# Kernel tuning notes

Measured on AMD Instinct MI355X. Metric: run time of the kernel, lower is better.

Reference implementation:

```python
import jax, jax.numpy as jnp
import numpy as np

N, C, H, W = 4, 128, 64, 64
HEADS, KS, RED = 4, 7, 18
D = C // HEADS


def _layernorm(x, w, b, eps=1e-5):
    mu = x.mean(axis=-1, keepdims=True)
    var = ((x - mu) ** 2).mean(axis=-1, keepdims=True)
    return (x - mu) * jax.lax.rsqrt(var + eps) * w + b


def _gelu(x):
    return jax.nn.gelu(x, approximate=False)


def setup_inputs() -> dict:
    key = jax.random.key(0)
    ks = jax.random.split(key, 16)
    s = 0.02
    inp = {
        'x': jax.random.normal(ks[0], (N, C, H, W), jnp.float32),
        'ln1_w': jnp.ones((C,), jnp.float32), 'ln1_b': jnp.zeros((C,), jnp.float32),
        'ln2_w': jnp.ones((C,), jnp.float32), 'ln2_b': jnp.zeros((C,), jnp.float32),
        'qkv_w': jax.random.normal(ks[1], (C, 3 * C), jnp.float32) * s,
        'qkv_b': jnp.zeros((3 * C,), jnp.float32),
        'proj_w': jax.random.normal(ks[2], (C, C), jnp.float32) * s,
        'proj_b': jnp.zeros((C,), jnp.float32),
        'rpb': jax.random.normal(ks[3], (HEADS, 2 * KS - 1, 2 * KS - 1), jnp.float32) * s,
        'conv1_w': jax.random.normal(ks[4], (C, C // 4), jnp.float32) * s,
        'conv1_b': jnp.zeros((C // 4,), jnp.float32),
        'conv2_w': jax.random.normal(ks[5], (C // 4, C), jnp.float32) * s,
        'conv2_b': jnp.zeros((C,), jnp.float32),
        'ca1_w': jax.random.normal(ks[6], (C, C // RED), jnp.float32) * s,
        'ca1_b': jnp.zeros((C // RED,), jnp.float32),
        'ca2_w': jax.random.normal(ks[7], (C // RED, C), jnp.float32) * s,
        'ca2_b': jnp.zeros((C,), jnp.float32),
        'fc1_w': jax.random.normal(ks[8], (C, 4 * C), jnp.float32) * s,
        'fc1_b': jnp.zeros((4 * C,), jnp.float32),
        'fc2_w': jax.random.normal(ks[9], (4 * C, C), jnp.float32) * s,
        'fc2_b': jnp.zeros((C,), jnp.float32),
    }
    return inp


def _na2d(xc, qkv_w, qkv_b, rpb, proj_w, proj_b):
    # xc: [N, H, W, C] -> neighborhood attention with clamped k x k windows (NATTEN semantics)
    n, h, w, c = xc.shape
    qkv = (xc @ qkv_w + qkv_b).reshape(n, h, w, 3, HEADS, D)
    q, k, v = qkv[..., 0, :, :], qkv[..., 1, :, :], qkv[..., 2, :, :]
    q = q * (D ** -0.5)
    half = KS // 2
    ni = jnp.clip(jnp.arange(h) - half, 0, h - KS)          # window start per query row
    nj = jnp.clip(jnp.arange(w) - half, 0, w - KS)
    idx_i = ni[:, None] + jnp.arange(KS)                     # [H, KS]
    idx_j = nj[:, None] + jnp.arange(KS)                     # [W, KS]
    # gather key/value windows: [N, H, KS, W, KS, heads, D]
    kw = k[:, idx_i][:, :, :, idx_j]
    vw = v[:, idx_i][:, :, :, idx_j]
    attn = jnp.einsum('nijhd,niajbhd->nijhab', q, kw)        # [N,H,W,heads,KS,KS]
    bi = idx_i - jnp.arange(h)[:, None] + (KS - 1)           # rel-pos bias row index [H,KS]
    bj = idx_j - jnp.arange(w)[:, None] + (KS - 1)           # [W,KS]
    bias = rpb[:, bi][:, :, :, bj]                           # [heads,H,KS,W,KS]
    attn = attn + bias.transpose(1, 3, 0, 2, 4)[None]        # -> [1,H,W,heads,KS,KS]
    attn = jax.nn.softmax(attn.reshape(n, h, w, HEADS, KS * KS), axis=-1)
    attn = attn.reshape(n, h, w, HEADS, KS, KS)
    out = jnp.einsum('nijhab,niajbhd->nijhd', attn, vw).reshape(n, h, w, c)
    return out @ proj_w + proj_b


def reference(x, ln1_w, ln1_b, ln2_w, ln2_b, qkv_w, qkv_b, proj_w, proj_b, rpb,
              conv1_w, conv1_b, conv2_w, conv2_b, ca1_w, ca1_b, ca2_w, ca2_b,
              fc1_w, fc1_b, fc2_w, fc2_b):
    n, c, h, w = x.shape
    xs = x.transpose(0, 2, 3, 1).reshape(n, h * w, c)        # n (h w) c
    shortcut = xs
    xn = _layernorm(xs, ln1_w, ln1_b)
    xc = xn.reshape(n, h, w, c)
    # conv branch: 1x1 -> GELU -> 1x1 -> channel attention
    t = _gelu(xc @ conv1_w + conv1_b) @ conv2_w + conv2_b
    g = t.mean(axis=(1, 2))                                  # global avg pool [N,C]
    g = jax.nn.sigmoid(jax.nn.relu(g @ ca1_w + ca1_b) @ ca2_w + ca2_b)
    ca_x = (t * g[:, None, None, :]).reshape(n, h * w, c)
    # neighborhood attention branch
    na_x = _na2d(xc, qkv_w, qkv_b, rpb, proj_w, proj_b).reshape(n, h * w, c)
    x2 = shortcut + na_x + ca_x * 0.02
    m = _gelu(_layernorm(x2, ln2_w, ln2_b) @ fc1_w + fc1_b) @ fc2_w + fc2_b
    x3 = x2 + m
    return x3.reshape(n, h, w, c).transpose(0, 3, 1, 2)
```

## Files before the change

### kernel.cpp

```cpp
#include <hip/hip_runtime.h>
#include <hip/hip_bf16.h>
#include <math.h>

#define NB 4
#define CC 128
#define HH 64
#define WW 64
#define HEADS 4
#define KS 7
#define DD 32
#define HW 4096
#define MTOT 16384

typedef unsigned short BF;
typedef short short8 __attribute__((ext_vector_type(8)));
typedef float floatx4 __attribute__((ext_vector_type(4)));

__device__ __forceinline__ float gelu_f(float x) {
    return 0.5f * x * (1.0f + erff(x * 0.70710678118654752440f));
}

__device__ __forceinline__ BF f2bf(float f) {
    union { float f; unsigned u; } a; a.f = f;
    unsigned u = a.u;
    unsigned r = u + 0x7FFFu + ((u >> 16) & 1u);
    return (BF)(r >> 16);
}

__device__ __forceinline__ float bf2f(BF v) {
    return __uint_as_float(((unsigned)v) << 16);
}

#define LDK 40
#define LDK128 136

__global__ __launch_bounds__(256) void ln1t_kernel(
    const float* __restrict__ x, const float* __restrict__ w,
    const float* __restrict__ b, BF* __restrict__ out,
    float* __restrict__ part,
    const float* __restrict__ qkv_w, const float* __restrict__ conv1_w,
    const float* __restrict__ conv2_w, const float* __restrict__ proj_w,
    const float* __restrict__ fc1_w, const float* __restrict__ fc2_w,
    BF* __restrict__ qkvT, BF* __restrict__ c1T, BF* __restrict__ c2T,
    BF* __restrict__ projT2, BF* __restrict__ fc1T2, BF* __restrict__ fc2T2)
{
    const int blk = blockIdx.x;
    const int t  = threadIdx.x;

    if (blk >= 512) {
        for (int idx = (blk - 512) * 256 + t; idx < 204800; idx += 32768) {
            if (idx < 49152) {
                int l = idx, n = l >> 7, k = l & 127;
                qkvT[l] = f2bf(qkv_w[k * 384 + n]);
            } else if (idx < 53248) {
                int l = idx - 49152, n = l >> 7, k = l & 127;
                c1T[l] = f2bf(conv1_w[k * 32 + n]);
            } else if (idx < 57344) {
                int l = idx - 53248, n = l >> 5, k = l & 31;
                c2T[l] = f2bf(conv2_w[k * 128 + n]);
            } else if (idx < 73728) {
                int l = idx - 57344, kk = l & 31, n = (l >> 5) & 127, ks = l >> 12;
                projT2[l] = f2bf(proj_w[(ks * 32 + kk) * 128 + n]);
            } else if (idx < 139264) {
                int l = idx - 73728, kk = l & 31, n = (l >> 5) & 511, ks = l >> 14;
                fc1T2[l] = f2bf(fc1_w[(ks * 32 + kk) * 512 + n]);
            } else {
                int l = idx - 139264, kk = l & 31, n = (l >> 5) & 127, ks = l >> 12;
                fc2T2[l] = f2bf(fc2_w[(ks * 32 + kk) * 128 + n]);
            }
        }
        return;
    }

    __shared__ float xt[128][33];
    __shared__ float mus[32], rss[32];
    const int n  = blk >> 7;
    const int p0 = (blk & 127) * 32;
    if (blk < 4 && t < 128) part[blk * CC + t] = 0.f;

    {
        int pp = t & 31, c8 = t >> 5;
        #pragma unroll 4
        for (int it = 0; it < 16; it++) {
            int c = it * 8 + c8;
            xt[c][pp] = x[(size_t)(n * CC + c) * HW + p0 + pp];
        }
    }
    __syncthreads();
    {
        int pp2 = t >> 3, cb = t & 7;
        float s = 0.f;
        #pragma unroll
        for (int u = 0; u < 16; u++) s += xt[cb + u * 8][pp2];
        s += __shfl_xor(s, 1); s += __shfl_xor(s, 2); s += __shfl_xor(s, 4);
        float mu = s * (1.0f / CC);
        float v = 0.f;
        #pragma unroll
        for (int u = 0; u < 16; u++) { float d = xt[cb + u * 8][pp2] - mu; v += d * d; }
        v += __shfl_xor(v, 1); v += __shfl_xor(v, 2); v += __shfl_xor(v, 4);
        if (cb == 0) { mus[pp2] = mu; rss[pp2] = rsqrtf(v * (1.0f / CC) + 1e-5f); }
    }
    __syncthreads();
    {
        #pragma unroll
        for (int it = 0; it < 2; it++) {
            int pp2 = (t >> 4) + it * 16;
            int c0  = (t & 15) * 8;
            float mu = mus[pp2], rs = rss[pp2];
            int m = n * HW + p0 + pp2;
            short8 o;
            #pragma unroll
            for (int u = 0; u < 8; u++)
                o[u] = (short)f2bf((xt[c0 + u][pp2] - mu) * rs * w[c0 + u] + b[c0 + u]);
            *(short8*)(out + (size_t)m * CC + c0) = o;
        }
    }
}

__global__ __launch_bounds__(256) void phase2(
    const BF* __restrict__ xn, const BF* __restrict__ qkvT,
    const float* __restrict__ qkv_b, BF* __restrict__ qkv_out,
    const BF* __restrict__ c1T, const float* __restrict__ b1,
    const BF* __restrict__ c2T, const float* __restrict__ b2,
    BF* __restrict__ tout, float* __restrict__ part)
{
    __shared__ __align__(16) char smem[26624];
    const int bid = blockIdx.x;
    const int t = threadIdx.x;
    const int w = t >> 6, lane = t & 63, q = lane >> 4, r16 = lane & 15;

    if (bid < 768) {
        BF* Bl = (BF*)smem;
        const int col0 = (bid % 6) * 64;
        const int row0 = (bid / 6) * 128;
        {
            int nn = t >> 2;
            int kk = (t & 3) * 32;
            const BF* src = qkvT + (size_t)(col0 + nn) * 128 + kk;
            #pragma unroll
            for (int u = 0; u < 4; u++)
                *(uint4*)(Bl + nn * LDK128 + kk + u * 8) = *(const uint4*)(src + u * 8);
        }
        __syncthreads();
        #pragma unroll
        for (int half = 0; half < 2; half++) {
            floatx4 acc[4] = {};
            const BF* arow = xn + (size_t)(row0 + half * 64 + w * 16 + r16) * CC;
            #pragma unroll
            for (int ks = 0; ks < 4; ks++) {
                short8 af = *(const short8*)(arow + ks * 32 + q * 8);
                #pragma unroll
                for (int nt = 0; nt < 4; nt++) {
                    short8 bf = *(const short8*)(Bl + (nt * 16 + r16) * LDK128 + ks * 32 + q * 8);
                    acc[nt] = __builtin_amdgcn_mfma_f32_16x16x32_bf16(af, bf, acc[nt], 0, 0, 0);
                }
            }
            #pragma unroll
            for (int nt = 0; nt < 4; nt++) {
                int col = col0 + nt * 16 + r16;
                float bv = qkv_b[col];
                #pragma unroll
                for (int reg = 0; reg < 4; reg++) {
                    int row = row0 + half * 64 + w * 16 + q * 4 + reg;
                    qkv_out[(size_t)row * 384 + col] = f2bf(acc[nt][reg] + bv);
                }
            }
        }
        return;
    }
    BF*    W1l = (BF*)smem;
    BF*    W2l = (BF*)(smem + 8704);
    BF*    Hl  = (BF*)(smem + 18944);
    float* red = (float*)(smem + 24064);
    const int row0 = (bid - 768) * 64;
    {
        #pragma unroll
        for (int it = 0; it < 2; it++) {
            int idx = it * 256 + t;
            int nn = idx >> 4, u = idx & 15;
            *(uint4*)(W1l + nn * LDK128 + u * 8) = *(const uint4*)(c1T + nn * 128 + u * 8);
        }
    }
    {
        #pragma unroll
        for (int it = 0; it < 2; it++) {
            int idx = it * 256 + t;
            int nn = idx >> 2, u = idx & 3;
            *(uint4*)(W2l + nn * LDK + u * 8) = *(const uint4*)(c2T + nn * 32 + u * 8);
        }
    }
    __syncthreads();
    floatx4 a1[2] = {};
    const BF* arow = xn + (size_t)(row0 + w * 16 + r16) * CC;
    #pragma unroll
    for (int ks = 0; ks < 4; ks++) {
        short8 af = *(const short8*)(arow + ks * 32 + q * 8);
        #pragma unroll
        for (int nt = 0; nt < 2; nt++) {
            short8 bf = *(const short8*)(W1l + (nt * 16 + r16) * LDK128 + ks * 32 + q * 8);
            a1[nt] = __builtin_amdgcn_mfma_f32_16x16x32_bf16(af, bf, a1[nt], 0, 0, 0);
        }
    }
    #pragma unroll
    for (int nt = 0; nt < 2; nt++) {
        int col = nt * 16 + r16;
        float bv = b1[col];
        #pragma unroll
        for (int reg = 0; reg < 4; reg++)
            Hl[(w * 16 + q * 4 + reg) * LDK + col] = f2bf(gelu_f(a1[nt][reg] + bv));
    }
    __syncthreads();
    floatx4 a2[8] = {};
    short8 af2 = *(const short8*)(Hl + (w * 16 + r16) * LDK + q * 8);
    #pragma unroll
    for (int nt = 0; nt < 8; nt++) {
        short8 bf = *(const short8*)(W2l + (nt * 16 + r16) * LDK + q * 8);
        a2[nt] = __builtin_amdgcn_mfma_f32_16x16x32_bf16(af2, bf, a2[nt], 0, 0, 0);
    }
    #pragma unroll
    for (int nt = 0; nt < 8; nt++) {
        int col = nt * 16 + r16;
        float bv = b2[col];
        float s = 0.f;
        #pragma unroll
        for (int reg = 0; reg < 4; reg++) {
            int row = row0 + w * 16 + q * 4 + reg;
            float v = a2[nt][reg] + bv;
            tout[(size_t)row * CC + col] = f2bf(v);
            s += v;
        }
        s += __shfl_xor(s, 16);
        s += __shfl_xor(s, 32);
        if (lane < 16) red[w * 128 + col] = s;
    }
    __syncthreads();
    if (t < 128) {
        float cs = red[t] + red[128 + t] + red[256 + t] + red[384 + t];
        atomicAdd(&part[(row0 >> 12) * CC + t], cs);
    }
}

__global__ __launch_bounds__(256) void na_mfma_kernel(
    const BF* __restrict__ qkv, const float* __restrict__ rpb,
    BF* __restrict__ outp)
{
    __shared__ __align__(16) BF Kt[224][40];
    __shared__ __align__(16) BF Vt[32][232];
    __shared__ __align__(16) BF Qb[64][40];
    __shared__ __align__(16) BF Pl[4][16][232];
    __shared__ float rb[169];

    const int b = blockIdx.x;
    const int h = b & 3;
    const int tile = b >> 2;
    const int n = tile >> 6;
    const int ti = (tile >> 3) & 7, tj = tile & 7;
    const int t = threadIdx.x;
    const int w = t >> 6, lane = t & 63, quad = lane >> 4, r16 = lane & 15;
    const int i0 = ti * 8, j0 = tj * 8;
    const int wi0 = max(i0 - 3, 0), wj0 = max(j0 - 3, 0);
    const int R  = min(wi0 + 13, 63) - wi0 + 1;
    const int Rj = min(wj0 + 13, 63) - wj0 + 1;

    for (int idx = t; idx < 896; idx += 256) {
        int key = idx >> 2, ch = idx & 3;
        int kr = key >> 4, kc = key & 15;
        uint4 v = {0u, 0u, 0u, 0u};
        if (kr < R && kc < Rj) {
            size_t pix = (size_t)((n * HH + wi0 + kr) * WW + wj0 + kc);
            v = *(const uint4*)(qkv + pix * 384 + 128 + h * DD + ch * 8);
        }
        *(uint4*)&Kt[key][ch * 8] = v;
    }
    for (int idx = t; idx < 896; idx += 256) {
        int key = idx >> 2, ch = idx & 3;
        int kr = key >> 4, kc = key & 15;
        if (kr < R && kc < Rj) {
            size_t pix = (size_t)((n * HH + wi0 + kr) * WW + wj0 + kc);
            uint4 v = *(const uint4*)(qkv + pix * 384 + 256 + h * DD + ch * 8);
            const BF* pv = (const BF*)&v;
            #pragma unroll
            for (int u = 0; u < 8; u++) Vt[ch * 8 + u][key] = pv[u];
        } else {
            #pragma unroll
            for (int u = 0; u < 8; u++) Vt[ch * 8 + u][key] = 0;
        }
    }
    {
        int q = t >> 2, ch = t & 3;
        size_t mq = (size_t)((n * HH + i0 + (q >> 3)) * WW + j0 + (q & 7));
        *(uint4*)&Qb[q][ch * 8] = *(const uint4*)(qkv + mq * 384 + h * DD + ch * 8);
    }
    if (t < 169) rb[t] = rpb[h * 169 + t];
    __syncthreads();

    int oi[4], cok[4], bj0[4], ai_[4];
    #pragma unroll
    for (int reg = 0; reg < 4; reg++) {
        int q = w * 16 + quad * 4 + reg;
        int i = i0 + (q >> 3), j = j0 + (q & 7);
        int ni = min(max(i - 3, 0), HH - KS), nj = min(max(j - 3, 0), WW - KS);
        oi[reg]  = ni - wi0;
        ai_[reg] = ni - i + 6;
        int dc = r16 - (nj - wj0);
        cok[reg] = ((unsigned)dc < 7u) ? 1 : 0;
        bj0[reg] = min(max(dc + (nj - j + 6), 0), 12);
    }

    short8 aq = *(const short8*)&Qb[w * 16 + r16][quad * 8];
    floatx4 S[14];
    #pragma unroll
    for (int nt = 0; nt < 14; nt++) {
        floatx4 z = {0.f, 0.f, 0.f, 0.f};
        short8 bk = *(const short8*)&Kt[nt * 16 + r16][quad * 8];
        S[nt] = __builtin_amdgcn_mfma_f32_16x16x32_bf16(aq, bk, z, 0, 0, 0);
    }
    const float scale = 0.17677669529663688110f;
    #pragma unroll
    for (int nt = 0; nt < 14; nt++) {
        #pragma unroll
        for (int reg = 0; reg < 4; reg++) {
            int dr = nt - oi[reg];
            bool ok = ((unsigned)dr < 7u) && cok[reg];
            int bi = min(max(dr + ai_[reg], 0), 12);
            float bias = rb[bi * 13 + bj0[reg]];
            S[nt][reg] = ok ? fmaf(S[nt][reg], scale, bias) : -1e30f;
        }
    }
    float rinv[4];
    #pragma unroll
    for (int reg = 0; reg < 4; reg++) {
        float m = S[0][reg];
        #pragma unroll
        for (int nt = 1; nt < 14; nt++) m = fmaxf(m, S[nt][reg]);
        m = fmaxf(m, __shfl_xor(m, 1));
        m = fmaxf(m, __shfl_xor(m, 2));
        m = fmaxf(m, __shfl_xor(m, 4));
        m = fmaxf(m, __shfl_xor(m, 8));
        float s = 0.f;
        #pragma unroll
        for (int nt = 0; nt < 14; nt++) {
            float e = __expf(S[nt][reg] - m);
            S[nt][reg] = e;
            s += e;
        }
        s += __shfl_xor(s, 1);
        s += __shfl_xor(s, 2);
        s += __shfl_xor(s, 4);
        s += __shfl_xor(s, 8);
        rinv[reg] = 1.0f / s;
    }
    #pragma unroll
    for (int nt = 0; nt < 14; nt++)
        #pragma unroll
        for (int reg = 0; reg < 4; reg++)
            Pl[w][quad * 4 + reg][nt * 16 + r16] = f2bf(S[nt][reg] * rinv[reg]);

    floatx4 O0 = {0.f, 0.f, 0.f, 0.f}, O1 = {0.f, 0.f, 0.f, 0.f};
    #pragma unroll
    for (int ks = 0; ks < 7; ks++) {
        short8 ap = *(const short8*)&Pl[w][r16][ks * 32 + quad * 8];
        short8 b0 = *(const short8*)&Vt[r16][ks * 32 + quad * 8];
        short8 b1 = *(const short8*)&Vt[16 + r16][ks * 32 + quad * 8];
        O0 = __builtin_amdgcn_mfma_f32_16x16x32_bf16(ap, b0, O0, 0, 0, 0);
        O1 = __builtin_amdgcn_mfma_f32_16x16x32_bf16(ap, b1, O1, 0, 0, 0);
    }
    #pragma unroll
    for (int reg = 0; reg < 4; reg++) {
        int q = w * 16 + quad * 4 + reg;
        size_t m = (size_t)((n * HH + i0 + (q >> 3)) * WW + j0 + (q & 7));
        outp[m * CC + h * DD + r16]      = f2bf(O0[reg]);
        outp[m * CC + h * DD + 16 + r16] = f2bf(O1[reg]);
    }
}

__global__ __launch_bounds__(256) void tail_kernel(
    const BF* __restrict__ A, const BF* __restrict__ projT2,
    const float* __restrict__ proj_b, const float* __restrict__ x,
    const BF* __restrict__ tbuf, const float* __restrict__ part,
    const float* __restrict__ ca1_w, const float* __restrict__ ca1_b,
    const float* __restrict__ ca2_w, const float* __restrict__ ca2_b,
    const float* __restrict__ w2, const float* __restrict__ b2,
    const BF* __restrict__ fc1T2, const float* __restrict__ fc1_b,
    const BF* __restrict__ fc2T2, const float* __restrict__ fc2_b,
    float* __restrict__ out)
{
    __shared__ float xs[32][132];
    __shared__ __align__(16) BF ln2l[32][136];
    __shared__ __align__(16) BF hl[32][520];
    __shared__ float st[128][34];
    __shared__ float gs[128], h1s[7], gl[128];
    __shared__ float S1[4][16], S2[4][16];

    const int t = threadIdx.x;
    const int w = t >> 6, lane = t & 63, quad = lane >> 4, r16 = lane & 15;
    const int row0 = blockIdx.x * 32;
    const int n = row0 >> 12, p0 = row0 & 4095;
    const int mt = w & 1, nh = w >> 1;
    const int lr0 = mt * 16;

    #pragma unroll
    for (int it = 0; it < 4; it++) {
        int idx4 = it * 256 + t;
        int p4 = idx4 & 7, c = idx4 >> 3;
        float4 v = *(const float4*)(x + (size_t)(n * CC + c) * HW + p0 + p4 * 4);
        xs[p4 * 4 + 0][c] = v.x; xs[p4 * 4 + 1][c] = v.y;
        xs[p4 * 4 + 2][c] = v.z; xs[p4 * 4 + 3][c] = v.w;
    }
    if (t < 128) gs[t] = part[n * CC + t] * (1.0f / HW);
    __syncthreads();
    if (t < 7) {
        float a = ca1_b[t];
        for (int k = 0; k < 128; k++) a += gs[k] * ca1_w[k * 7 + t];
        h1s[t] = fmaxf(a, 0.f);
    }
    __syncthreads();
    if (t < 128) {
        float o = ca2_b[t];
        #pragma unroll
        for (int r = 0; r < 7; r++) o += h1s[r] * ca2_w[r * 128 + t];
        gl[t] = 1.0f / (1.0f + expf(-o));
    }

    floatx4 acc[4] = {};
    const BF* arow = A + (size_t)(row0 + lr0 + r16) * CC;
    #pragma unroll
    for (int ks = 0; ks < 4; ks++) {
        short8 af = *(const short8*)(arow + ks * 32 + quad * 8);
        #pragma unroll
        for (int nt = 0; nt < 4; nt++) {
            int col = nh * 64 + nt * 16 + r16;
            short8 bf = *(const short8*)(projT2 + ((size_t)(ks * 128 + col)) * 32 + quad * 8);
            acc[nt] = __builtin_amdgcn_mfma_f32_16x16x32_bf16(af, bf, acc[nt], 0, 0, 0);
        }
    }
    __syncthreads();

    float x2r[4][4];
    float s1[4] = {0.f, 0.f, 0.f, 0.f}, s2[4] = {0.f, 0.f, 0.f, 0.f};
    #pragma unroll
    for (int nt = 0; nt < 4; nt++) {
        int col = nh * 64 + nt * 16 + r16;
        float bv = proj_b[col], gv = gl[col];
        #pragma unroll
        for (int reg = 0; reg < 4; reg++) {
            int lr = lr0 + quad * 4 + reg;
            float tv = bf2f(tbuf[(size_t)(row0 + lr) * CC + col]);
            float v = acc[nt][reg] + bv + xs[lr][col] + 0.02f * tv * gv;
            x2r[nt][reg] = v;
            s1[reg] += v; s2[reg] += v * v;
        }
    }
    #pragma unroll
    for (int reg = 0; reg < 4; reg++) {
        #pragma unroll
        for (int off = 8; off; off >>= 1) {
            s1[reg] += __shfl_xor(s1[reg], off);
            s2[reg] += __shfl_xor(s2[reg], off);
        }
    }
    if (r16 == 0) {
        #pragma unroll
        for (int reg = 0; reg < 4; reg++) {
            S1[w][quad * 4 + reg] = s1[reg];
            S2[w][quad * 4 + reg] = s2[reg];
        }
    }
    __syncthreads();
    const int pw = w ^ 2;
    float mu[4], rr[4];
    #pragma unroll
    for (int reg = 0; reg < 4; reg++) {
        int r = quad * 4 + reg;
        float t1 = S1[w][r] + S1[pw][r];
        float t2 = S2[w][r] + S2[pw][r];
        mu[reg] = t1 * (1.0f / CC);
        float var = t2 * (1.0f / CC) - mu[reg] * mu[reg];
        rr[reg] = rsqrtf(var + 1e-5f);
    }
    #pragma unroll
    for (int nt = 0; nt < 4; nt++) {
        int col = nh * 64 + nt * 16 + r16;
        float wv = w2[col], bv2 = b2[col];
        #pragma unroll
        for (int reg = 0; reg < 4; reg++) {
            int lr = lr0 + quad * 4 + reg;
            ln2l[lr][col] = f2bf((x2r[nt][reg] - mu[reg]) * rr[reg] * wv + bv2);
        }
    }
    __syncthreads();

    short8 af1[4];
    #pragma unroll
    for (int ks = 0; ks < 4; ks++)
        af1[ks] = *(const short8*)&ln2l[lr0 + r16][ks * 32 + quad * 8];
    #pragma unroll
    for (int g = 0; g < 4; g++) {
        floatx4 a2[4] = {};
        #pragma unroll
        for (int ks = 0; ks < 4; ks++) {
            #pragma unroll
            for (int nt = 0; nt < 4; nt++) {
                int col = nh * 256 + g * 64 + nt * 16 + r16;
                short8 bf = *(const short8*)(fc1T2 + ((size_t)(ks * 512 + col)) * 32 + quad * 8);
                a2[nt] = __builtin_amdgcn_mfma_f32_16x16x32_bf16(af1[ks], bf, a2[nt], 0, 0, 0);
            }
        }
        #pragma unroll
        for (int nt = 0; nt < 4; nt++) {
            int col = nh * 256 + g * 64 + nt * 16 + r16;
            float bv = fc1_b[col];
            #pragma unroll
            for (int reg = 0; reg < 4; reg++) {
                int lr = lr0 + quad * 4 + reg;
                hl[lr][col] = f2bf(gelu_f(a2[nt][reg] + bv));
            }
        }
    }
    __syncthreads();

    floatx4 a3[4] = {};
    #pragma unroll
    for (int ks = 0; ks < 16; ks++) {
        short8 af = *(const short8*)&hl[lr0 + r16][ks * 32 + quad * 8];
        #pragma unroll
        for (int nt = 0; nt < 4; nt++) {
            int col = nh * 64 + nt * 16 + r16;
            short8 bf = *(const short8*)(fc2T2 + ((size_t)(ks * 128 + col)) * 32 + quad * 8);
            a3[nt] = __builtin_amdgcn_mfma_f32_16x16x32_bf16(af, bf, a3[nt], 0, 0, 0);
        }
    }
    #pragma unroll
    for (int nt = 0; nt < 4; nt++) {
        int col = nh * 64 + nt * 16 + r16;
        float bv = fc2_b[col];
        #pragma unroll
        for (int reg = 0; reg < 4; reg++) {
            int lr = lr0 + quad * 4 + reg;
            st[col][lr] = a3[nt][reg] + bv + x2r[nt][reg];
        }
    }
    __syncthreads();
    {
        int col = t >> 1, ch = (t & 1) * 16;
        float* dst = out + (size_t)(n * CC + col) * HW + p0 + ch;
        #pragma unroll
        for (int u = 0; u < 4; u++) {
            float4 v;
            v.x = st[col][ch + u * 4 + 0];
            v.y = st[col][ch + u * 4 + 1];
            v.z = st[col][ch + u * 4 + 2];
            v.w = st[col][ch + u * 4 + 3];
            *(float4*)(dst + u * 4) = v;
        }
    }
}

extern "C" void kernel_launch(void* const* d_in, const int* in_sizes, int n_in,
                              void* d_out, int out_size, void* d_ws, size_t ws_size,
                              hipStream_t stream)
{
    const float* x       = (const float*)d_in[0];
    const float* ln1_w   = (const float*)d_in[1];
    const float* ln1_b   = (const float*)d_in[2];
    const float* ln2_w   = (const float*)d_in[3];
    const float* ln2_b   = (const float*)d_in[4];
    const float* qkv_w   = (const float*)d_in[5];
    const float* qkv_b   = (const float*)d_in[6];
    const float* proj_w  = (const float*)d_in[7];
    const float* proj_b  = (const float*)d_in[8];
    const float* rpb     = (const float*)d_in[9];
    const float* conv1_w = (const float*)d_in[10];
    const float* conv1_b = (const float*)d_in[11];
    const float* conv2_w = (const float*)d_in[12];
    const float* conv2_b = (const float*)d_in[13];
    const float* ca1_w   = (const float*)d_in[14];
    const float* ca1_b   = (const float*)d_in[15];
    const float* ca2_w   = (const float*)d_in[16];
    const float* ca2_b   = (const float*)d_in[17];
    const float* fc1_w   = (const float*)d_in[18];
    const float* fc1_b   = (const float*)d_in[19];
    const float* fc2_w   = (const float*)d_in[20];
    const float* fc2_b   = (const float*)d_in[21];
    float* out = (float*)d_out;

    char* ws = (char*)d_ws;
    BF*    xn_bf   = (BF*)(ws);
    BF*    qkv_bf  = (BF*)(ws + 4194304);
    BF*    t_bf    = (BF*)(ws + 16777216);
    BF*    na_bf   = (BF*)(ws + 20971520);
    float* part    = (float*)(ws + 25165824);
    BF*    qkvT    = (BF*)(ws + 25167872);
    BF*    c1T     = (BF*)(ws + 25266176);
    BF*    c2T     = (BF*)(ws + 25274368);
    BF*    projT2  = (BF*)(ws + 25282560);
    BF*    fc1T2   = (BF*)(ws + 25315328);
    BF*    fc2T2   = (BF*)(ws + 25446400);

    ln1t_kernel<<<640, 256, 0, stream>>>(x, ln1_w, ln1_b, xn_bf, part,
        qkv_w, conv1_w, conv2_w, proj_w, fc1_w, fc2_w,
        qkvT, c1T, c2T, projT2, fc1T2, fc2T2);
    phase2<<<1024, 256, 0, stream>>>(xn_bf, qkvT, qkv_b, qkv_bf,
                                     c1T, conv1_b, c2T, conv2_b, t_bf, part);
    na_mfma_kernel<<<1024, 256, 0, stream>>>(qkv_bf, rpb, na_bf);
    tail_kernel<<<512, 256, 0, stream>>>(na_bf, projT2, proj_b, x, t_bf, part,
                                         ca1_w, ca1_b, ca2_w, ca2_b,
                                         ln2_w, ln2_b, fc1T2, fc1_b,
                                         fc2T2, fc2_b, out);
}
```

Before: 171.0 us.

## Skip out-of-window key tiles in NA and shrink tail tiles for occupancy

In the neighborhood attention kernel, each wave now computes QK scores for only the 8 key-row tiles its queries can reach instead of all 14. It zeroes the adjacent padding tiles and runs 4–5 PV steps instead of 7, cutting MFMA, softmax and LDS work. The tail kernel moves to 16-row blocks with twice as many blocks. Its four waves split the columns rather than forming a 2x2 grid, and the xs/st buffers share one LDS region. This lowers LDS and register use to raise occupancy, at the cost of re-reading weight tiles more often and an extra barrier.

```diff
diff --git a/kernel.cpp b/kernel.cpp
--- a/kernel.cpp
+++ b/kernel.cpp
@@ -294,6 +294,8 @@
     if (t < 169) rb[t] = rpb[h * 169 + t];
     __syncthreads();
 
+    const int kt0 = min(max(i0 + 2 * w - 3, 0), HH - KS) - wi0;
+
     int oi[4], cok[4], bj0[4], ai_[4];
     #pragma unroll
     for (int reg = 0; reg < 4; reg++) {
@@ -308,23 +310,23 @@
     }
 
     short8 aq = *(const short8*)&Qb[w * 16 + r16][quad * 8];
-    floatx4 S[14];
-    #pragma unroll
-    for (int nt = 0; nt < 14; nt++) {
+    floatx4 S[8];
+    #pragma unroll
+    for (int jt = 0; jt < 8; jt++) {
         floatx4 z = {0.f, 0.f, 0.f, 0.f};
-        short8 bk = *(const short8*)&Kt[nt * 16 + r16][quad * 8];
-        S[nt] = __builtin_amdgcn_mfma_f32_16x16x32_bf16(aq, bk, z, 0, 0, 0);
+        short8 bk = *(const short8*)&Kt[(kt0 + jt) * 16 + r16][quad * 8];
+        S[jt] = __builtin_amdgcn_mfma_f32_16x16x32_bf16(aq, bk, z, 0, 0, 0);
     }
     const float scale = 0.17677669529663688110f;
     #pragma unroll
-    for (int nt = 0; nt < 14; nt++) {
-        #pragma unroll
-        for (int reg = 0; reg < 4; reg++) {
-            int dr = nt - oi[reg];
+    for (int jt = 0; jt < 8; jt++) {
+        #pragma unroll
+        for (int reg = 0; reg < 4; reg++) {
+            int dr = kt0 + jt - oi[reg];
             bool ok = ((unsigned)dr < 7u) && cok[reg];
             int bi = min(max(dr + ai_[reg], 0), 12);
             float bias = rb[bi * 13 + bj0[reg]];
-            S[nt][reg] = ok ? fmaf(S[nt][reg], scale, bias) : -1e30f;
+            S[jt][reg] = ok ? fmaf(S[jt][reg], scale, bias) : -1e30f;
         }
     }
     float rinv[4];
@@ -332,16 +334,16 @@
     for (int reg = 0; reg < 4; reg++) {
         float m = S[0][reg];
         #pragma unroll
-        for (int nt = 1; nt < 14; nt++) m = fmaxf(m, S[nt][reg]);
+        for (int jt = 1; jt < 8; jt++) m = fmaxf(m, S[jt][reg]);
         m = fmaxf(m, __shfl_xor(m, 1));
         m = fmaxf(m, __shfl_xor(m, 2));
         m = fmaxf(m, __shfl_xor(m, 4));
         m = fmaxf(m, __shfl_xor(m, 8));
         float s = 0.f;
         #pragma unroll
-        for (int nt = 0; nt < 14; nt++) {
-            float e = __expf(S[nt][reg] - m);
-            S[nt][reg] = e;
+        for (int jt = 0; jt < 8; jt++) {
+            float e = __expf(S[jt][reg] - m);
+            S[jt][reg] = e;
             s += e;
         }
         s += __shfl_xor(s, 1);
@@ -351,19 +353,31 @@
         rinv[reg] = 1.0f / s;
     }
     #pragma unroll
-    for (int nt = 0; nt < 14; nt++)
+    for (int jt = 0; jt < 8; jt++)
         #pragma unroll
         for (int reg = 0; reg < 4; reg++)
-            Pl[w][quad * 4 + reg][nt * 16 + r16] = f2bf(S[nt][reg] * rinv[reg]);
-
+            Pl[w][quad * 4 + reg][(kt0 + jt) * 16 + r16] = f2bf(S[jt][reg] * rinv[reg]);
+    if (kt0 & 1) {
+        #pragma unroll
+        for (int reg = 0; reg < 4; reg++) {
+            Pl[w][quad * 4 + reg][(kt0 - 1) * 16 + r16] = 0;
+            Pl[w][quad * 4 + reg][(kt0 + 8) * 16 + r16] = 0;
+        }
+    }
+
+    const int ks0 = kt0 >> 1;
+    const int nch = 4 + (kt0 & 1);
     floatx4 O0 = {0.f, 0.f, 0.f, 0.f}, O1 = {0.f, 0.f, 0.f, 0.f};
     #pragma unroll
-    for (int ks = 0; ks < 7; ks++) {
-        short8 ap = *(const short8*)&Pl[w][r16][ks * 32 + quad * 8];
-        short8 b0 = *(const short8*)&Vt[r16][ks * 32 + quad * 8];
-        short8 b1 = *(const short8*)&Vt[16 + r16][ks * 32 + quad * 8];
-        O0 = __builtin_amdgcn_mfma_f32_16x16x32_bf16(ap, b0, O0, 0, 0, 0);
-        O1 = __builtin_amdgcn_mfma_f32_16x16x32_bf16(ap, b1, O1, 0, 0, 0);
+    for (int c2 = 0; c2 < 5; c2++) {
+        if (c2 < nch) {
+            int ks = ks0 + c2;
+            short8 ap = *(const short8*)&Pl[w][r16][ks * 32 + quad * 8];
+            short8 b0 = *(const short8*)&Vt[r16][ks * 32 + quad * 8];
+            short8 b1 = *(const short8*)&Vt[16 + r16][ks * 32 + quad * 8];
+            O0 = __builtin_amdgcn_mfma_f32_16x16x32_bf16(ap, b0, O0, 0, 0, 0);
+            O1 = __builtin_amdgcn_mfma_f32_16x16x32_bf16(ap, b1, O1, 0, 0, 0);
+        }
     }
     #pragma unroll
     for (int reg = 0; reg < 4; reg++) {
@@ -385,27 +399,27 @@
     const BF* __restrict__ fc2T2, const float* __restrict__ fc2_b,
     float* __restrict__ out)
 {
-    __shared__ float xs[32][132];
-    __shared__ __align__(16) BF ln2l[32][136];
-    __shared__ __align__(16) BF hl[32][520];
-    __shared__ float st[128][34];
-    __shared__ float gs[128], h1s[7], gl[128];
+    __shared__ __align__(16) char sarena[9216];
+    __shared__ __align__(16) BF ln2l[16][136];
+    __shared__ __align__(16) BF hl[16][520];
+    __shared__ float gs[128], h1s[8], gl[128];
     __shared__ float S1[4][16], S2[4][16];
+
+    float* xs = (float*)sarena;
+    float* st = (float*)sarena;
 
     const int t = threadIdx.x;
     const int w = t >> 6, lane = t & 63, quad = lane >> 4, r16 = lane & 15;
-    const int row0 = blockIdx.x * 32;
+    const int row0 = blockIdx.x * 16;
     const int n = row0 >> 12, p0 = row0 & 4095;
-    const int mt = w & 1, nh = w >> 1;
-    const int lr0 = mt * 16;
-
-    #pragma unroll
-    for (int it = 0; it < 4; it++) {
+
+    #pragma unroll
+    for (int it = 0; it < 2; it++) {
         int idx4 = it * 256 + t;
-        int p4 = idx4 & 7, c = idx4 >> 3;
+        int p4 = idx4 & 3, c = idx4 >> 2;
         float4 v = *(const float4*)(x + (size_t)(n * CC + c) * HW + p0 + p4 * 4);
-        xs[p4 * 4 + 0][c] = v.x; xs[p4 * 4 + 1][c] = v.y;
-        xs[p4 * 4 + 2][c] = v.z; xs[p4 * 4 + 3][c] = v.w;
+        xs[(p4 * 4 + 0) * 132 + c] = v.x; xs[(p4 * 4 + 1) * 132 + c] = v.y;
+        xs[(p4 * 4 + 2) * 132 + c] = v.z; xs[(p4 * 4 + 3) * 132 + c] = v.w;
     }
     if (t < 128) gs[t] = part[n * CC + t] * (1.0f / HW);
     __syncthreads();
@@ -422,31 +436,31 @@
         gl[t] = 1.0f / (1.0f + expf(-o));
     }
 
-    floatx4 acc[4] = {};
-    const BF* arow = A + (size_t)(row0 + lr0 + r16) * CC;
+    floatx4 acc[2] = {};
+    const BF* arow = A + (size_t)(row0 + r16) * CC;
     #pragma unroll
     for (int ks = 0; ks < 4; ks++) {
         short8 af = *(const short8*)(arow + ks * 32 + quad * 8);
         #pragma unroll
-        for (int nt = 0; nt < 4; nt++) {
-            int col = nh * 64 + nt * 16 + r16;
+        for (int nt = 0; nt < 2; nt++) {
+            int col = w * 32 + nt * 16 + r16;
             short8 bf = *(const short8*)(projT2 + ((size_t)(ks * 128 + col)) * 32 + quad * 8);
             acc[nt] = __builtin_amdgcn_mfma_f32_16x16x32_bf16(af, bf, acc[nt], 0, 0, 0);
         }
     }
     __syncthreads();
 
-    float x2r[4][4];
+    float x2r[2][4];
     float s1[4] = {0.f, 0.f, 0.f, 0.f}, s2[4] = {0.f, 0.f, 0.f, 0.f};
     #pragma unroll
-    for (int nt = 0; nt < 4; nt++) {
-        int col = nh * 64 + nt * 16 + r16;
+    for (int nt = 0; nt < 2; nt++) {
+        int col = w * 32 + nt * 16 + r16;
         float bv = proj_b[col], gv = gl[col];
         #pragma unroll
         for (int reg = 0; reg < 4; reg++) {
-            int lr = lr0 + quad * 4 + reg;
+            int lr = quad * 4 + reg;
             float tv = bf2f(tbuf[(size_t)(row0 + lr) * CC + col]);
-            float v = acc[nt][reg] + bv + xs[lr][col] + 0.02f * tv * gv;
+            float v = acc[nt][reg] + bv + xs[lr * 132 + col] + 0.02f * tv * gv;
             x2r[nt][reg] = v;
             s1[reg] += v; s2[reg] += v * v;
         }
@@ -454,7 +468,7 @@
     #pragma unroll
     for (int reg = 0; reg < 4; reg++) {
         #pragma unroll
-        for (int off = 8; off; off >>= 1) {
+        for (int off = 1; off < 16; off <<= 1) {
             s1[reg] += __shfl_xor(s1[reg], off);
             s2[reg] += __shfl_xor(s2[reg], off);
         }
@@ -467,24 +481,23 @@
         }
     }
     __syncthreads();
-    const int pw = w ^ 2;
     float mu[4], rr[4];
     #pragma unroll
     for (int reg = 0; reg < 4; reg++) {
         int r = quad * 4 + reg;
-        float t1 = S1[w][r] + S1[pw][r];
-        float t2 = S2[w][r] + S2[pw][r];
+        float t1 = S1[0][r] + S1[1][r] + S1[2][r] + S1[3][r];
+        float t2 = S2[0][r] + S2[1][r] + S2[2][r] + S2[3][r];
         mu[reg] = t1 * (1.0f / CC);
         float var = t2 * (1.0f / CC) - mu[reg] * mu[reg];
         rr[reg] = rsqrtf(var + 1e-5f);
     }
     #pragma unroll
-    for (int nt = 0; nt < 4; nt++) {
-        int col = nh * 64 + nt * 16 + r16;
+    for (int nt = 0; nt < 2; nt++) {
+        int col = w * 32 + nt * 16 + r16;
         float wv = w2[col], bv2 = b2[col];
         #pragma unroll
         for (int reg = 0; reg < 4; reg++) {
-            int lr = lr0 + quad * 4 + reg;
+            int lr = quad * 4 + reg;
             ln2l[lr][col] = f2bf((x2r[nt][reg] - mu[reg]) * rr[reg] * wv + bv2);
         }
     }
@@ -493,64 +506,62 @@
     short8 af1[4];
     #pragma unroll
     for (int ks = 0; ks < 4; ks++)
-        af1[ks] = *(const short8*)&ln2l[lr0 + r16][ks * 32 + quad * 8];
-    #pragma unroll
-    for (int g = 0; g < 4; g++) {
-        floatx4 a2[4] = {};
-        #pragma unroll
-        for (int ks = 0; ks < 4; ks++) {
-            #pragma unroll
-            for (int nt = 0; nt < 4; nt++) {
-                int col = nh * 256 + g * 64 + nt * 16 + r16;
-                short8 bf = *(const short8*)(fc1T2 + ((size_t)(ks * 512 + col)) * 32 + quad * 8);
-                a2[nt] = __builtin_amdgcn_mfma_f32_16x16x32_bf16(af1[ks], bf, a2[nt], 0, 0, 0);
-            }
-        }
-        #pragma unroll
-        for (int nt = 0; nt < 4; nt++) {
-            int col = nh * 256 + g * 64 + nt * 16 + r16;
-            float bv = fc1_b[col];
-            #pragma unroll
-            for (int reg = 0; reg < 4; reg++) {
-                int lr = lr0 + quad * 4 + reg;
-                hl[lr][col] = f2bf(gelu_f(a2[nt][reg] + bv));
-            }
-        }
-    }
-    __syncthreads();
-
-    floatx4 a3[4] = {};
+        af1[ks] = *(const short8*)&ln2l[r16][ks * 32 + quad * 8];
+    floatx4 a2[8] = {};
+    #pragma unroll
+    for (int ks = 0; ks < 4; ks++) {
+        #pragma unroll
+        for (int nt = 0; nt < 8; nt++) {
+            int col = w * 128 + nt * 16 + r16;
+            short8 bf = *(const short8*)(fc1T2 + ((size_t)(ks * 512 + col)) * 32 + quad * 8);
+            a2[nt] = __builtin_amdgcn_mfma_f32_16x16x32_bf16(af1[ks], bf, a2[nt], 0, 0, 0);
+        }
+    }
+    #pragma unroll
+    for (int nt = 0; nt < 8; nt++) {
+        int col = w * 128 + nt * 16 + r16;
+        float bv = fc1_b[col];
+        #pragma unroll
+        for (int reg = 0; reg < 4; reg++) {
+            int lr = quad * 4 + reg;
+            hl[lr][col] = f2bf(gelu_f(a2[nt][reg] + bv));
+        }
+    }
+    __syncthreads();
+
+    floatx4 a3[2] = {};
     #pragma unroll
     for (int ks = 0; ks < 16; ks++) {
-        short8 af = *(const short8*)&hl[lr0 + r16][ks * 32 + quad * 8];
-        #pragma unroll
-        for (int nt = 0; nt < 4; nt++) {
-            int col = nh * 64 + nt * 16 + r16;
+        short8 af = *(const short8*)&hl[r16][ks * 32 + quad * 8];
+        #pragma unroll
+        for (int nt = 0; nt < 2; nt++) {
+            int col = w * 32 + nt * 16 + r16;
             short8 bf = *(const short8*)(fc2T2 + ((size_t)(ks * 128 + col)) * 32 + quad * 8);
             a3[nt] = __builtin_amdgcn_mfma_f32_16x16x32_bf16(af, bf, a3[nt], 0, 0, 0);
         }
     }
-    #pragma unroll
-    for (int nt = 0; nt < 4; nt++) {
-        int col = nh * 64 + nt * 16 + r16;
+    __syncthreads();
+    #pragma unroll
+    for (int nt = 0; nt < 2; nt++) {
+        int col = w * 32 + nt * 16 + r16;
         float bv = fc2_b[col];
         #pragma unroll
         for (int reg = 0; reg < 4; reg++) {
-            int lr = lr0 + quad * 4 + reg;
-            st[col][lr] = a3[nt][reg] + bv + x2r[nt][reg];
+            int lr = quad * 4 + reg;
+            st[col * 18 + lr] = a3[nt][reg] + bv + x2r[nt][reg];
         }
     }
     __syncthreads();
     {
-        int col = t >> 1, ch = (t & 1) * 16;
-        float* dst = out + (size_t)(n * CC + col) * HW + p0 + ch;
-        #pragma unroll
-        for (int u = 0; u < 4; u++) {
+        int col = t >> 1, half = t & 1;
+        float* dst = out + (size_t)(n * CC + col) * HW + p0 + half * 8;
+        #pragma unroll
+        for (int u = 0; u < 2; u++) {
             float4 v;
-            v.x = st[col][ch + u * 4 + 0];
-            v.y = st[col][ch + u * 4 + 1];
-            v.z = st[col][ch + u * 4 + 2];
-            v.w = st[col][ch + u * 4 + 3];
+            v.x = st[col * 18 + half * 8 + u * 4 + 0];
+            v.y = st[col * 18 + half * 8 + u * 4 + 1];
+            v.z = st[col * 18 + half * 8 + u * 4 + 2];
+            v.w = st[col * 18 + half * 8 + u * 4 + 3];
             *(float4*)(dst + u * 4) = v;
         }
     }
@@ -603,8 +614,8 @@
     phase2<<<1024, 256, 0, stream>>>(xn_bf, qkvT, qkv_b, qkv_bf,
                                      c1T, conv1_b, c2T, conv2_b, t_bf, part);
     na_mfma_kernel<<<1024, 256, 0, stream>>>(qkv_bf, rpb, na_bf);
-    tail_kernel<<<512, 256, 0, stream>>>(na_bf, projT2, proj_b, x, t_bf, part,
-                                         ca1_w, ca1_b, ca2_w, ca2_b,
-                                         ln2_w, ln2_b, fc1T2, fc1_b,
-                                         fc2T2, fc2_b, out);
-}
+    tail_kernel<<<1024, 256, 0, stream>>>(na_bf, projT2, proj_b, x, t_bf, part,
+                                          ca1_w, ca1_b, ca2_w, ca2_b,
+                                          ln2_w, ln2_b, fc1T2, fc1_b,
+                                          fc2T2, fc2_b, out);
+}
```

Result: faster. 162.8 us (-4.8%).
